# Kernel tuning notes

Measured on AMD Instinct MI355X. Metric: run time of the kernel, lower is better.

## Reference

```python
import jax, jax.numpy as jnp
import numpy as np

DN = ('NCHW', 'OIHW', 'NCHW')

def conv2d(x, w, b, stride, pad):
    y = jax.lax.conv_general_dilated(x, w, (stride, stride), ((pad, pad), (pad, pad)), dimension_numbers=DN)
    return y + b[None, :, None, None]

def convt2d(x, w, b):
    # torch ConvTranspose2d(k=4, stride=2, padding=1); torch weight layout [Cin, Cout, kH, kW]
    wf = jnp.flip(w, (2, 3)).transpose(1, 0, 2, 3)  # -> [Cout, Cin, kH, kW]
    y = jax.lax.conv_general_dilated(x, wf, (1, 1), ((2, 2), (2, 2)), lhs_dilation=(2, 2), dimension_numbers=DN)
    return y + b[None, :, None, None]

def setup_inputs() -> dict:
    key = jax.random.key(0)
    ks = jax.random.split(key, 20)
    Hc, E, K = 128, 256, 8192
    s = lambda k, shape, fan: jax.random.normal(k, shape, jnp.float32) * (1.0 / np.sqrt(fan))
    inp = {
        'x': jax.random.normal(ks[0], (4, 3, 256, 256), jnp.float32),
        'enc_w1': s(ks[1], (Hc, 3, 4, 4), 3 * 16), 'enc_b1': jnp.zeros((Hc,), jnp.float32),
        'enc_w2': s(ks[2], (Hc, Hc, 4, 4), Hc * 16), 'enc_b2': jnp.zeros((Hc,), jnp.float32),
        'enc_w3': s(ks[3], (Hc, Hc, 3, 3), Hc * 9), 'enc_b3': jnp.zeros((Hc,), jnp.float32),
        'qconv_w': s(ks[4], (E, Hc, 1, 1), Hc), 'qconv_b': jnp.zeros((E,), jnp.float32),
        'codebook': jax.random.uniform(ks[5], (K, E), jnp.float32, -1.0 / K, 1.0 / K),
        'pqconv_w': s(ks[6], (Hc, E, 1, 1), E), 'pqconv_b': jnp.zeros((Hc,), jnp.float32),
        'dec_w1': s(ks[7], (Hc, Hc, 3, 3), Hc * 9), 'dec_b1': jnp.zeros((Hc,), jnp.float32),
        'dect_w2': s(ks[8], (Hc, Hc, 4, 4), Hc * 16), 'dect_b2': jnp.zeros((Hc,), jnp.float32),
        'dect_w3': s(ks[9], (Hc, 3, 4, 4), Hc * 16), 'dect_b3': jnp.zeros((3,), jnp.float32),
    }
    return inp

def quantize(z, codebook):
    B, C, H, W = z.shape
    zf = z.transpose(0, 2, 3, 1).reshape(-1, C)  # [N, C]
    d = (jnp.sum(zf * zf, axis=1, keepdims=True)
         + jnp.sum(codebook * codebook, axis=1)
         - 2.0 * zf @ codebook.T)  # [N, K]
    indices = jnp.argmin(d, axis=1)
    quant = codebook[indices].reshape(B, H, W, C).transpose(0, 3, 1, 2)
    commit_loss = jnp.mean((jax.lax.stop_gradient(quant) - z) ** 2)
    quant = z + jax.lax.stop_gradient(quant - z)  # straight-through
    return quant, indices, commit_loss

def reference(x, enc_w1, enc_b1, enc_w2, enc_b2, enc_w3, enc_b3, qconv_w, qconv_b,
              codebook, pqconv_w, pqconv_b, dec_w1, dec_b1, dect_w2, dect_b2, dect_w3, dect_b3):
    h = jax.nn.relu(conv2d(x, enc_w1, enc_b1, 2, 1))
    h = jax.nn.relu(conv2d(h, enc_w2, enc_b2, 2, 1))
    h = conv2d(h, enc_w3, enc_b3, 1, 1)
    h = conv2d(h, qconv_w, qconv_b, 1, 0)
    quant, indices, commit_loss = quantize(h, codebook)
    q = conv2d(quant, pqconv_w, pqconv_b, 1, 0)
    d = jax.nn.relu(conv2d(q, dec_w1, dec_b1, 1, 1))
    d = jax.nn.relu(convt2d(d, dect_w2, dect_b2))
    recon = convt2d(d, dect_w3, dect_b3)
    return recon, commit_loss, indices
```

## Files before the change

### kernel.cpp

```cpp
#include <hip/hip_runtime.h>

#define OFF_A     ((size_t)0)
#define OFF_BINFO ((size_t)8388608)
#define OFF_B     ((size_t)34611200)
#define OFF_C     ((size_t)43532288)
#define OFF_D     ((size_t)52453376)
#define OFF_E     ((size_t)69230592)
#define OFF_ZN    ((size_t)81813504)
#define OFF_CN    ((size_t)81879040)
#define OFF_IDX   ((size_t)81911808)
#define OFF_ACC   ((size_t)81977344)
#define OFF_WR2   ((size_t)81977600)
#define OFF_WR3   ((size_t)83026176)
#define OFF_QWT   ((size_t)83050752)
#define OFF_WD2   ((size_t)83181824)
#define OFF_WD3   ((size_t)85278976)
#define OFF_WD1   ((size_t)86458624)

#define VQ_MARGIN 1.2e-4f
#define LDSS 40

typedef __attribute__((ext_vector_type(8))) _Float16 f16x8;
typedef __attribute__((ext_vector_type(4))) float f32x4;

__device__ __forceinline__ unsigned fkey(float f) {
  unsigned u = __float_as_uint(f);
  return (u & 0x80000000u) ? ~u : (u | 0x80000000u);
}
__device__ __forceinline__ float funkey(unsigned k) {
  unsigned u = (k & 0x80000000u) ? (k ^ 0x80000000u) : ~k;
  return __uint_as_float(u);
}
__device__ __forceinline__ void padzero_img(float* base, int S, int t) {
  for (int e = t; e < 4 * S - 4; e += 256) {
    int rr, cc;
    if (e < S) { rr = 0; cc = e; }
    else if (e < 2 * S) { rr = S - 1; cc = e - S; }
    else { rr = ((e - 2 * S) >> 1) + 1; cc = (e & 1) ? (S - 1) : 0; }
    base[rr * S + cc] = 0.0f;
  }
}

__global__ __launch_bounds__(256) void prep_k(
    const float* __restrict__ dtw2, float* __restrict__ wr2,
    const float* __restrict__ dtw3, float* __restrict__ wr3,
    const float* __restrict__ qw,   float* __restrict__ qwT,
    const float* __restrict__ ew2,  double* __restrict__ wd2,
    const float* __restrict__ ew3,  double* __restrict__ wd3,
    const float* __restrict__ ew1,  double* __restrict__ wd1,
    float* __restrict__ xpad, float* __restrict__ h1p, float* __restrict__ h2p) {
  int b = blockIdx.x, t = threadIdx.x;
  if (b < 256) {
    int tid = b * 256 + t;
    int ci = tid & 127, co = (tid >> 7) & 127, cls = tid >> 14;
    int kh0 = 1 - (cls >> 1), kw0 = 1 - (cls & 1);
    const float* s = dtw2 + ((size_t)ci * 128 + co) * 16;
    float* d = wr2 + (size_t)tid * 4;
    d[0] = s[kh0 * 4 + kw0];       d[1] = s[kh0 * 4 + kw0 + 2];
    d[2] = s[(kh0 + 2) * 4 + kw0]; d[3] = s[(kh0 + 2) * 4 + kw0 + 2];
  } else if (b < 262) {
    int tid = (b - 256) * 256 + t;
    if (tid < 1536) {
      int ci = tid & 127, co = (tid >> 7) % 3, cls = tid / 384;
      int kh0 = 1 - (cls >> 1), kw0 = 1 - (cls & 1);
      const float* s = dtw3 + ((size_t)ci * 3 + co) * 16;
      float* d = wr3 + (size_t)tid * 4;
      d[0] = s[kh0 * 4 + kw0];       d[1] = s[kh0 * 4 + kw0 + 2];
      d[2] = s[(kh0 + 2) * 4 + kw0]; d[3] = s[(kh0 + 2) * 4 + kw0 + 2];
    }
  } else if (b < 390) {
    int tid = (b - 262) * 256 + t;
    int co = tid & 255, ci = tid >> 8;
    qwT[(size_t)ci * 256 + co] = qw[(size_t)co * 128 + ci];
  } else if (b < 1414) {
    int tid = (b - 390) * 256 + t;
    wd2[tid] = (double)ew2[tid];
  } else if (b < 1990) {
    int tid = (b - 1414) * 256 + t;
    wd3[tid] = (double)ew3[tid];
  } else if (b < 2014) {
    int tid = (b - 1990) * 256 + t;
    wd1[tid] = (double)ew1[tid];
  } else if (b < 2026) {
    padzero_img(xpad + (size_t)(b - 2014) * 66564, 258, t);
  } else if (b < 2538) {
    padzero_img(h1p + (size_t)(b - 2026) * 16900, 130, t);
  } else {
    padzero_img(h2p + (size_t)(b - 2538) * 4356, 66, t);
  }
}

__global__ __launch_bounds__(256) void padx_k(const float* __restrict__ x,
                                              float* __restrict__ xp) {
  int tid = blockIdx.x * 256 + threadIdx.x;
  int wo = tid & 255, ho = (tid >> 8) & 255, c = tid >> 16;
  xp[((size_t)c * 258 + ho + 1) * 258 + wo + 1] = x[tid];
}

__global__ __launch_bounds__(256) void conv1_k(
    const float* __restrict__ xp, const double* __restrict__ wd,
    const float* __restrict__ bias, float* __restrict__ h1p) {
  int b = blockIdx.x;
  int chunk = b & 63, cog = (b >> 6) & 31, n = b >> 11;
  int t = threadIdx.x;
  int wo = t & 127, ho = chunk * 2 + (t >> 7);
  int co0 = cog * 4;
  const float* xb = xp + (size_t)n * 3 * 66564 + (size_t)(2 * ho) * 258 + 2 * wo;
  double acc[4] = {0.0, 0.0, 0.0, 0.0};
  for (int ci = 0; ci < 3; ++ci) {
    const float* xc = xb + (size_t)ci * 66564;
    double xd[16];
#pragma unroll
    for (int kh = 0; kh < 4; ++kh)
#pragma unroll
      for (int kw = 0; kw < 4; ++kw) xd[kh * 4 + kw] = (double)xc[kh * 258 + kw];
#pragma unroll
    for (int cc = 0; cc < 4; ++cc) {
      const double* wp = wd + (size_t)(co0 + cc) * 48 + ci * 16;
#pragma unroll
      for (int tp = 0; tp < 16; ++tp)
        acc[cc] = fma(xd[tp], wp[tp], acc[cc]);
    }
  }
#pragma unroll
  for (int cc = 0; cc < 4; ++cc) {
    float r = (float)((double)bias[co0 + cc] + acc[cc]);
    h1p[(((size_t)n * 128 + co0 + cc) * 130 + ho + 1) * 130 + wo + 1] = fmaxf(r, 0.0f);
  }
}

__global__ __launch_bounds__(256) void conv2_k(
    const float* __restrict__ h1p, const double* __restrict__ wd,
    const float* __restrict__ bias, float* __restrict__ h2p) {
  int b = blockIdx.x;
  int chunk = b & 15, cog = (b >> 4) & 31, n = b >> 9;
  int t = threadIdx.x;
  int wo = t & 63, ho = chunk * 4 + (t >> 6);
  int co0 = cog * 4;
  const float* xb = h1p + (size_t)n * 128 * 16900 + (size_t)(2 * ho) * 130 + 2 * wo;
  double acc[4] = {0.0, 0.0, 0.0, 0.0};
  for (int ci = 0; ci < 128; ++ci) {
    const float* xc = xb + (size_t)ci * 16900;
    double xd[16];
#pragma unroll
    for (int kh = 0; kh < 4; ++kh)
#pragma unroll
      for (int kw = 0; kw < 4; ++kw) xd[kh * 4 + kw] = (double)xc[kh * 130 + kw];
#pragma unroll
    for (int cc = 0; cc < 4; ++cc) {
      const double* wp = wd + (size_t)(co0 + cc) * 2048 + ci * 16;
#pragma unroll
      for (int tp = 0; tp < 16; ++tp)
        acc[cc] = fma(xd[tp], wp[tp], acc[cc]);
    }
  }
#pragma unroll
  for (int cc = 0; cc < 4; ++cc) {
    float r = (float)((double)bias[co0 + cc] + acc[cc]);
    h2p[(((size_t)n * 128 + co0 + cc) * 66 + ho + 1) * 66 + wo + 1] = fmaxf(r, 0.0f);
  }
}

__global__ __launch_bounds__(256) void conv3_k(
    const float* __restrict__ h2p, const double* __restrict__ wd,
    const float* __restrict__ bias, float* __restrict__ h3) {
  int b = blockIdx.x;
  int chunk = b & 15, cog = (b >> 4) & 31, n = b >> 9;
  int t = threadIdx.x;
  int wo = t & 63, ho = chunk * 4 + (t >> 6);
  int co0 = cog * 4;
  const float* xb = h2p + (size_t)n * 128 * 4356 + (size_t)ho * 66 + wo;
  double acc[4] = {0.0, 0.0, 0.0, 0.0};
  for (int ci = 0; ci < 128; ++ci) {
    const float* xc = xb + (size_t)ci * 4356;
    double xd[9];
#pragma unroll
    for (int kh = 0; kh < 3; ++kh)
#pragma unroll
      for (int kw = 0; kw < 3; ++kw) xd[kh * 3 + kw] = (double)xc[kh * 66 + kw];
#pragma unroll
    for (int cc = 0; cc < 4; ++cc) {
      const double* wp = wd + (size_t)(co0 + cc) * 1152 + ci * 9;
#pragma unroll
      for (int tp = 0; tp < 9; ++tp)
        acc[cc] = fma(xd[tp], wp[tp], acc[cc]);
    }
  }
#pragma unroll
  for (int cc = 0; cc < 4; ++cc)
    h3[(((size_t)n * 128 + co0 + cc) << 12) + (ho << 6) + wo] =
        (float)((double)bias[co0 + cc] + acc[cc]);
}

__global__ __launch_bounds__(256) void qconv_z_k(
    const float* __restrict__ h3, const float* __restrict__ wT,
    const float* __restrict__ bias, float* __restrict__ zf,
    _Float16* __restrict__ Ap, float* __restrict__ znb) {
  __shared__ double wsum[4];
  int p  = blockIdx.x;
  int co = threadIdx.x;
  int n  = p >> 12;
  int hw = p & 4095;
  const float* xp = h3 + ((size_t)n * 128) * 4096 + hw;
  double a[4] = {0.0, 0.0, 0.0, 0.0};
  for (int ci = 0; ci < 128; ci += 4) {
#pragma unroll
    for (int u = 0; u < 4; ++u) {
      float xv = xp[(size_t)(ci + u) * 4096];
      a[u] = fma((double)xv, (double)wT[(size_t)(ci + u) * 256 + co], a[u]);
    }
  }
  double acc = (double)bias[co] + ((a[0] + a[1]) + (a[2] + a[3]));
  float zv = (float)acc;
  zf[(size_t)p * 256 + co] = zv;
  Ap[(size_t)p * 256 + co] = (_Float16)zv;
  float xx = zv * zv;
  double s = (double)xx;
#pragma unroll
  for (int off = 32; off > 0; off >>= 1) s += __shfl_down(s, off, 64);
  if ((co & 63) == 0) wsum[co >> 6] = s;
  __syncthreads();
  if (co == 0) znb[p] = (float)((wsum[0] + wsum[1]) + (wsum[2] + wsum[3]));
}

__global__ __launch_bounds__(256) void cbprep_k(
    const float* __restrict__ cb, _Float16* __restrict__ Bp,
    float* __restrict__ cnb) {
  __shared__ double wsum[4];
  int k = blockIdx.x, t = threadIdx.x;
  float c = cb[(size_t)k * 256 + t];
  Bp[(size_t)k * 256 + t] = (_Float16)(c * 512.0f);
  float xx = c * c;
  double s = (double)xx;
#pragma unroll
  for (int off = 32; off > 0; off >>= 1) s += __shfl_down(s, off, 64);
  if ((t & 63) == 0) wsum[t >> 6] = s;
  __syncthreads();
  if (t == 0) cnb[k] = (float)((wsum[0] + wsum[1]) + (wsum[2] + wsum[3]));
}

__global__ __launch_bounds__(256, 2) void vq_gemm_k(
    const _Float16* __restrict__ Ah, const _Float16* __restrict__ Bh,
    const float* __restrict__ cnArr, int4* __restrict__ binfo) {
  __shared__ __align__(16) _Float16 As[128 * LDSS];
  __shared__ __align__(16) _Float16 Bs[128 * LDSS];
  __shared__ unsigned loc[128];
  __shared__ int cnt_sh[128];
  __shared__ int cand_sh[128][2];
  const int t = threadIdx.x;
  const int w = t >> 6, L = t & 63;
  const int mb = blockIdx.x >> 6;
  const int nb = blockIdx.x & 63;
  const int m0 = mb << 7, n0 = nb << 7;
  if (t < 128) { loc[t] = 0xFFFFFFFFu; cnt_sh[t] = 0; }
  f32x4 acc[4][4] = {};
  const int wr = (w >> 1) << 6, wc = (w & 1) << 6;
  const int srow = L >> 2, kg = L & 3;
  const int q = L >> 4, ln = L & 15;
  for (int kk = 0; kk < 256; kk += 32) {
    __syncthreads();
#pragma unroll
    for (int c = 0; c < 2; ++c) {
      const int row = (w << 5) + (c << 4) + srow;
      const f16x8 av = *(const f16x8*)(Ah + (size_t)(m0 + row) * 256 + kk + kg * 8);
      *(f16x8*)(&As[row * LDSS + kg * 8]) = av;
      const f16x8 bv = *(const f16x8*)(Bh + (size_t)(n0 + row) * 256 + kk + kg * 8);
      *(f16x8*)(&Bs[row * LDSS + kg * 8]) = bv;
    }
    __syncthreads();
    f16x8 af[4], bf[4];
#pragma unroll
    for (int i = 0; i < 4; ++i)
      af[i] = *(const f16x8*)(&As[(wr + 16 * i + ln) * LDSS + q * 8]);
#pragma unroll
    for (int j = 0; j < 4; ++j)
      bf[j] = *(const f16x8*)(&Bs[(wc + 16 * j + ln) * LDSS + q * 8]);
#pragma unroll
    for (int i = 0; i < 4; ++i)
#pragma unroll
      for (int j = 0; j < 4; ++j)
        acc[i][j] = __builtin_amdgcn_mfma_f32_16x16x32_f16(af[i], bf[j], acc[i][j], 0, 0, 0);
  }
  float cnv[4];
#pragma unroll
  for (int j = 0; j < 4; ++j) cnv[j] = cnArr[n0 + wc + 16 * j + ln];
#pragma unroll
  for (int i = 0; i < 4; ++i)
#pragma unroll
    for (int r = 0; r < 4; ++r) {
      float mn = 3.4e38f;
#pragma unroll
      for (int j = 0; j < 4; ++j)
        mn = fminf(mn, fmaf(-0.00390625f, acc[i][j][r], cnv[j]));
      atomicMin(&loc[wr + 16 * i + 4 * q + r], fkey(mn));
    }
  __syncthreads();
#pragma unroll
  for (int i = 0; i < 4; ++i)
#pragma unroll
    for (int r = 0; r < 4; ++r) {
      const int rib = wr + 16 * i + 4 * q + r;
      const float thr = funkey(loc[rib]) + VQ_MARGIN;
#pragma unroll
      for (int j = 0; j < 4; ++j) {
        float s = fmaf(-0.00390625f, acc[i][j][r], cnv[j]);
        if (s <= thr) {
          int slot = atomicAdd(&cnt_sh[rib], 1);
          if (slot < 2) cand_sh[rib][slot] = n0 + wc + 16 * j + ln;
        }
      }
    }
  __syncthreads();
  if (t < 128) {
    int4 v;
    v.x = cnt_sh[t];
    v.y = cand_sh[t][0];
    v.z = cand_sh[t][1];
    v.w = (int)__float_as_uint(funkey(loc[t]));
    binfo[(size_t)(m0 + t) * 64 + nb] = v;
  }
}

__global__ __launch_bounds__(256) void vq_phase3_k(
    const float* __restrict__ zf, const float* __restrict__ cb,
    const float* __restrict__ znArr, const float* __restrict__ cnArr,
    const int4* __restrict__ binfo, int* __restrict__ idxOut,
    float* __restrict__ accum) {
  if (blockIdx.x == 0 && threadIdx.x == 0) *accum = 0.0f;
  const int lane = threadIdx.x & 63;
  const int r = blockIdx.x * 4 + (threadIdx.x >> 6);
  const float* zr = zf + (size_t)r * 256;
  double z4[4];
#pragma unroll
  for (int j = 0; j < 4; ++j) z4[j] = (double)zr[lane + (j << 6)];
  const float znr = znArr[r];
  int4 b = binfo[(size_t)r * 64 + lane];
  float bv = __uint_as_float((unsigned)b.w);
  float m = bv;
#pragma unroll
  for (int off = 32; off > 0; off >>= 1) m = fminf(m, __shfl_down(m, off, 64));
  m = __shfl(m, 0, 64);
  const float thr = m + VQ_MARGIN;
  unsigned long long mask = __ballot(bv <= thr);
  float bestd = 3.4e38f;
  int bestk = 0x7fffffff;
  while (mask) {
    const int nb = (int)__builtin_ctzll(mask);
    mask &= mask - 1;
    const int c  = __shfl(b.x, nb, 64);
    const int k0 = __shfl(b.y, nb, 64);
    const int k1 = __shfl(b.z, nb, 64);
    const int nsc = (c <= 2) ? c : 128;
    for (int s2 = 0; s2 < nsc; ++s2) {
      const int k = (c <= 2) ? (s2 == 0 ? k0 : k1) : (nb * 128 + s2);
      const float* ck = cb + (size_t)k * 256;
      double p = 0.0;
#pragma unroll
      for (int j = 0; j < 4; ++j)
        p = fma(z4[j], (double)ck[lane + (j << 6)], p);
#pragma unroll
      for (int off = 32; off > 0; off >>= 1) p += __shfl_down(p, off, 64);
      if (lane == 0) {
        float mm2 = (float)(2.0 * p);
        float t1 = znr + cnArr[k];
        float d = t1 - mm2;
        if (d < bestd || (d == bestd && k < bestk)) { bestd = d; bestk = k; }
      }
    }
  }
  if (lane == 0) idxOut[r] = bestk;
}

__global__ __launch_bounds__(256) void commit_k(
    const float* __restrict__ zf, const float* __restrict__ cb,
    const int* __restrict__ idxArr, float* __restrict__ accum,
    float* __restrict__ outIdxF) {
  __shared__ float wsum[4];
  const int p = blockIdx.x;
  const int t = threadIdx.x;
  const int k = idxArr[p];
  float d = cb[(size_t)k * 256 + t] - zf[(size_t)p * 256 + t];
  float v = d * d;
#pragma unroll
  for (int off = 32; off > 0; off >>= 1) v += __shfl_down(v, off, 64);
  if ((t & 63) == 0) wsum[t >> 6] = v;
  __syncthreads();
  if (t == 0) {
    atomicAdd(accum, wsum[0] + wsum[1] + wsum[2] + wsum[3]);
    outIdxF[p] = (float)k;
  }
}

__global__ __launch_bounds__(256) void pc_k(const float* __restrict__ cb,
                                            const float* __restrict__ pw,
                                            float* __restrict__ PC) {
  int tid = blockIdx.x * 256 + threadIdx.x;
  int co = tid & 127, k = tid >> 7;
  const float* c = cb + (size_t)k * 256;
  const float* w = pw + (size_t)co * 256;
  float a0 = 0.0f, a1 = 0.0f, a2 = 0.0f, a3 = 0.0f;
  for (int ci = 0; ci < 256; ci += 4) {
    a0 = fmaf(c[ci], w[ci], a0);
    a1 = fmaf(c[ci + 1], w[ci + 1], a1);
    a2 = fmaf(c[ci + 2], w[ci + 2], a2);
    a3 = fmaf(c[ci + 3], w[ci + 3], a3);
  }
  PC[tid] = (a0 + a1) + (a2 + a3);
}

__global__ __launch_bounds__(256) void padzero_dec_k(
    float* __restrict__ qbufp, float* __restrict__ d1p, float* __restrict__ d2p) {
  int b = blockIdx.x, t = threadIdx.x;
  if (b < 512)       padzero_img(qbufp + (size_t)b * 4356, 66, t);
  else if (b < 1024) padzero_img(d1p + (size_t)(b - 512) * 4356, 66, t);
  else               padzero_img(d2p + (size_t)(b - 1024) * 16900, 130, t);
}

__global__ __launch_bounds__(256) void gather_pc_k(
    const float* __restrict__ PC, const int* __restrict__ idxArr,
    const float* __restrict__ pb, float* __restrict__ qp) {
  int tid = blockIdx.x * 256 + threadIdx.x;
  int hw = tid & 4095;
  int co = (tid >> 12) & 127;
  int n  = tid >> 19;
  int p  = (n << 12) + hw;
  int h = hw >> 6, w2 = hw & 63;
  qp[(((size_t)n * 128 + co) * 66 + h + 1) * 66 + w2 + 1] =
      PC[(size_t)idxArr[p] * 128 + co] + pb[co];
}

__global__ __launch_bounds__(256) void dconv1_k(
    const float* __restrict__ qp, const float* __restrict__ w,
    const float* __restrict__ bias, float* __restrict__ d1p) {
  int b = blockIdx.x;
  int chunk = b & 15, cog = (b >> 4) & 31, n = b >> 9;
  int t = threadIdx.x;
  int wo = t & 63, ho = chunk * 4 + (t >> 6);
  int co0 = cog * 4;
  const float* xb = qp + (size_t)n * 128 * 4356 + (size_t)ho * 66 + wo;
  float acc[4] = {0.0f, 0.0f, 0.0f, 0.0f};
  for (int ci = 0; ci < 128; ++ci) {
    const float* xc = xb + (size_t)ci * 4356;
    float xv[9];
#pragma unroll
    for (int kh = 0; kh < 3; ++kh)
#pragma unroll
      for (int kw = 0; kw < 3; ++kw) xv[kh * 3 + kw] = xc[kh * 66 + kw];
#pragma unroll
    for (int cc = 0; cc < 4; ++cc) {
      const float* wp = w + (size_t)(co0 + cc) * 1152 + ci * 9;
#pragma unroll
      for (int tp = 0; tp < 9; ++tp)
        acc[cc] = fmaf(xv[tp], wp[tp], acc[cc]);
    }
  }
#pragma unroll
  for (int cc = 0; cc < 4; ++cc)
    d1p[(((size_t)n * 128 + co0 + cc) * 66 + ho + 1) * 66 + wo + 1] =
        fmaxf(bias[co0 + cc] + acc[cc], 0.0f);
}

__global__ __launch_bounds__(256) void convt2_k(
    const float* __restrict__ xp, const float* __restrict__ wr,
    const float* __restrict__ bias, float* __restrict__ y) {
  int b = blockIdx.x;
  int chunk = b & 15, cls = (b >> 4) & 3, cog = (b >> 6) & 31, n = b >> 11;
  int cph = cls >> 1, cpw = cls & 1;
  int t = threadIdx.x;
  int wb = t & 63, i = chunk * 4 + (t >> 6);
  int co0 = cog * 4;
  int ho = 2 * i + cph, wo = 2 * wb + cpw;
  int r0 = i + 1 + cph, r1 = r0 - 1;
  int c0 = wb + 1 + cpw, c1 = c0 - 1;
  const float* xb = xp + (size_t)n * 128 * 4356;
  float acc[4] = {0.0f, 0.0f, 0.0f, 0.0f};
  for (int ci = 0; ci < 128; ++ci) {
    const float* xc = xb + (size_t)ci * 4356;
    float x00 = xc[r0 * 66 + c0], x01 = xc[r0 * 66 + c1];
    float x10 = xc[r1 * 66 + c0], x11 = xc[r1 * 66 + c1];
#pragma unroll
    for (int cc = 0; cc < 4; ++cc) {
      const float* w4 = wr + (((size_t)cls * 128 + co0 + cc) * 128 + ci) * 4;
      acc[cc] = fmaf(x00, w4[0], acc[cc]);
      acc[cc] = fmaf(x01, w4[1], acc[cc]);
      acc[cc] = fmaf(x10, w4[2], acc[cc]);
      acc[cc] = fmaf(x11, w4[3], acc[cc]);
    }
  }
#pragma unroll
  for (int cc = 0; cc < 4; ++cc)
    y[(((size_t)n * 128 + co0 + cc) * 130 + ho + 1) * 130 + wo + 1] =
        fmaxf(bias[co0 + cc] + acc[cc], 0.0f);
}

__global__ __launch_bounds__(256) void convt3_k(
    const float* __restrict__ xp, const float* __restrict__ wr,
    const float* __restrict__ bias, float* __restrict__ y,
    const float* __restrict__ accum, float* __restrict__ outLoss) {
  int b = blockIdx.x;
  if (b == 0 && threadIdx.x == 0) *outLoss = *accum * (1.0f / 4194304.0f);
  int chunk = b & 63, cls = (b >> 6) & 3, n = b >> 8;
  int cph = cls >> 1, cpw = cls & 1;
  int t = threadIdx.x;
  int wb = t & 127, i = chunk * 2 + (t >> 7);
  int ho = 2 * i + cph, wo = 2 * wb + cpw;
  int r0 = i + 1 + cph, r1 = r0 - 1;
  int c0 = wb + 1 + cpw, c1 = c0 - 1;
  const float* xb = xp + (size_t)n * 128 * 16900;
  float acc[3] = {0.0f, 0.0f, 0.0f};
  for (int ci = 0; ci < 128; ++ci) {
    const float* xc = xb + (size_t)ci * 16900;
    float x00 = xc[r0 * 130 + c0], x01 = xc[r0 * 130 + c1];
    float x10 = xc[r1 * 130 + c0], x11 = xc[r1 * 130 + c1];
#pragma unroll
    for (int cc = 0; cc < 3; ++cc) {
      const float* w4 = wr + (((size_t)cls * 3 + cc) * 128 + ci) * 4;
      acc[cc] = fmaf(x00, w4[0], acc[cc]);
      acc[cc] = fmaf(x01, w4[1], acc[cc]);
      acc[cc] = fmaf(x10, w4[2], acc[cc]);
      acc[cc] = fmaf(x11, w4[3], acc[cc]);
    }
  }
#pragma unroll
  for (int cc = 0; cc < 3; ++cc)
    y[(((size_t)n * 3 + cc) << 16) + (ho << 8) + wo] = bias[cc] + acc[cc];
}

extern "C" void kernel_launch(void* const* d_in, const int* in_sizes, int n_in,
                              void* d_out, int out_size, void* d_ws, size_t ws_size,
                              hipStream_t stream) {
  const float* x    = (const float*)d_in[0];
  const float* ew1  = (const float*)d_in[1];
  const float* eb1  = (const float*)d_in[2];
  const float* ew2  = (const float*)d_in[3];
  const float* eb2  = (const float*)d_in[4];
  const float* ew3  = (const float*)d_in[5];
  const float* eb3  = (const float*)d_in[6];
  const float* qw   = (const float*)d_in[7];
  const float* qb   = (const float*)d_in[8];
  const float* cb   = (const float*)d_in[9];
  const float* pw   = (const float*)d_in[10];
  const float* pb   = (const float*)d_in[11];
  const float* dw1  = (const float*)d_in[12];
  const float* db1  = (const float*)d_in[13];
  const float* dtw2 = (const float*)d_in[14];
  const float* dtb2 = (const float*)d_in[15];
  const float* dtw3 = (const float*)d_in[16];
  const float* dtb3 = (const float*)d_in[17];

  char* wsb = (char*)d_ws;
  float*    h1p  = (float*)(wsb + OFF_A);
  _Float16* Ap   = (_Float16*)(wsb + OFF_A);
  int4*     binfo= (int4*)(wsb + OFF_BINFO);
  float*    d2p  = (float*)(wsb + OFF_A);
  float*    h2p  = (float*)(wsb + OFF_B);
  float*    qbufp= (float*)(wsb + OFF_B);
  float*    xpad = (float*)(wsb + OFF_C);
  float*    h3   = (float*)(wsb + OFF_C);
  float*    d1p  = (float*)(wsb + OFF_C);
  float*    zff  = (float*)(wsb + OFF_D);
  _Float16* Bp   = (_Float16*)(wsb + OFF_E);
  float*    PC   = (float*)(wsb + OFF_E);
  float*    znb  = (float*)(wsb + OFF_ZN);
  float*    cnb  = (float*)(wsb + OFF_CN);
  int*      idxb = (int*)(wsb + OFF_IDX);
  float*    accum= (float*)(wsb + OFF_ACC);
  float*    wr2  = (float*)(wsb + OFF_WR2);
  float*    wr3  = (float*)(wsb + OFF_WR3);
  float*    qwT  = (float*)(wsb + OFF_QWT);
  double*   wd2  = (double*)(wsb + OFF_WD2);
  double*   wd3  = (double*)(wsb + OFF_WD3);
  double*   wd1  = (double*)(wsb + OFF_WD1);

  float* out      = (float*)d_out;
  float* outLoss  = out + 786432;
  float* outIdxF  = out + 786433;

  hipLaunchKernelGGL(prep_k, dim3(3050), dim3(256), 0, stream,
                     dtw2, wr2, dtw3, wr3, qw, qwT, ew2, wd2, ew3, wd3,
                     ew1, wd1, xpad, h1p, h2p);

  hipLaunchKernelGGL(padx_k,    dim3(3072),  dim3(256), 0, stream, x, xpad);
  hipLaunchKernelGGL(conv1_k,   dim3(8192),  dim3(256), 0, stream, xpad, wd1, eb1, h1p);
  hipLaunchKernelGGL(conv2_k,   dim3(2048),  dim3(256), 0, stream, h1p, wd2, eb2, h2p);
  hipLaunchKernelGGL(conv3_k,   dim3(2048),  dim3(256), 0, stream, h2p, wd3, eb3, h3);
  hipLaunchKernelGGL(qconv_z_k, dim3(16384), dim3(256), 0, stream, h3, qwT, qb, zff, Ap, znb);

  hipLaunchKernelGGL(cbprep_k,    dim3(8192),  dim3(256), 0, stream, cb, Bp, cnb);
  hipLaunchKernelGGL(vq_gemm_k,   dim3(8192),  dim3(256), 0, stream, Ap, Bp, cnb, binfo);
  hipLaunchKernelGGL(vq_phase3_k, dim3(4096),  dim3(256), 0, stream, zff, cb, znb, cnb, binfo, idxb, accum);
  hipLaunchKernelGGL(commit_k,    dim3(16384), dim3(256), 0, stream, zff, cb, idxb, accum, outIdxF);

  hipLaunchKernelGGL(pc_k,          dim3(4096), dim3(256), 0, stream, cb, pw, PC);
  hipLaunchKernelGGL(padzero_dec_k, dim3(1536), dim3(256), 0, stream, qbufp, d1p, d2p);
  hipLaunchKernelGGL(gather_pc_k,   dim3(8192), dim3(256), 0, stream, PC, idxb, pb, qbufp);
  hipLaunchKernelGGL(dconv1_k,      dim3(2048), dim3(256), 0, stream, qbufp, dw1, db1, d1p);
  hipLaunchKernelGGL(convt2_k,      dim3(8192), dim3(256), 0, stream, d1p, wr2, dtb2, d2p);
  hipLaunchKernelGGL(convt3_k,      dim3(1024), dim3(256), 0, stream, d2p, wr3, dtb3, out, accum, outLoss);
}
```

Measured before the change: 1.540 ms.

## Prefetch conv inputs, interleave weights by output group, and remap blocks per XCD

Double-precision encoder weights are rearranged so the four output channels of a group sit next to each other, letting each input value feed four contiguous weight loads. The direct-conv kernels (conv2, conv3, dconv1, convt2, convt3) now software-prefetch the next input channel's patch into registers while computing the current one. Block indices are remapped so blocks sharing the same spatial tile land on the same XCD for L2 reuse, and launch bounds request 4 blocks per CU. The cost is higher register pressure from the prefetch buffers, which may cause spills or lower occupancy under the min-blocks hint.

Result: slower. 1.603 ms (+4.0%).

```diff
diff --git a/kernel.cpp b/kernel.cpp
--- a/kernel.cpp
+++ b/kernel.cpp
@@ -74,13 +74,18 @@
     qwT[(size_t)ci * 256 + co] = qw[(size_t)co * 128 + ci];
   } else if (b < 1414) {
     int tid = (b - 390) * 256 + t;
-    wd2[tid] = (double)ew2[tid];
+    int co = tid >> 11, ci = (tid >> 4) & 127, tp = tid & 15;
+    wd2[((((size_t)(co >> 2) * 128 + ci) * 16 + tp) << 2) + (co & 3)] = (double)ew2[tid];
   } else if (b < 1990) {
     int tid = (b - 1414) * 256 + t;
-    wd3[tid] = (double)ew3[tid];
+    int co = tid / 1152, rem = tid - co * 1152;
+    int ci = rem / 9, tp = rem - ci * 9;
+    wd3[((((size_t)(co >> 2) * 128 + ci) * 9 + tp) << 2) + (co & 3)] = (double)ew3[tid];
   } else if (b < 2014) {
     int tid = (b - 1990) * 256 + t;
-    wd1[tid] = (double)ew1[tid];
+    int co = tid / 48, rem = tid - co * 48;
+    int ci = rem >> 4, tp = rem & 15;
+    wd1[((((size_t)(co >> 2) * 3 + ci) * 16 + tp) << 2) + (co & 3)] = (double)ew1[tid];
   } else if (b < 2026) {
     padzero_img(xpad + (size_t)(b - 2014) * 66564, 258, t);
   } else if (b < 2538) {
@@ -97,7 +102,7 @@
   xp[((size_t)c * 258 + ho + 1) * 258 + wo + 1] = x[tid];
 }
 
-__global__ __launch_bounds__(256) void conv1_k(
+__global__ __launch_bounds__(256, 4) void conv1_k(
     const float* __restrict__ xp, const double* __restrict__ wd,
     const float* __restrict__ bias, float* __restrict__ h1p) {
   int b = blockIdx.x;
@@ -106,22 +111,26 @@
   int wo = t & 127, ho = chunk * 2 + (t >> 7);
   int co0 = cog * 4;
   const float* xb = xp + (size_t)n * 3 * 66564 + (size_t)(2 * ho) * 258 + 2 * wo;
-  double acc[4] = {0.0, 0.0, 0.0, 0.0};
+  const double* wb = wd + (size_t)cog * 192;
+  float cf[48];
+#pragma unroll
   for (int ci = 0; ci < 3; ++ci) {
     const float* xc = xb + (size_t)ci * 66564;
-    double xd[16];
 #pragma unroll
     for (int kh = 0; kh < 4; ++kh)
 #pragma unroll
-      for (int kw = 0; kw < 4; ++kw) xd[kh * 4 + kw] = (double)xc[kh * 258 + kw];
-#pragma unroll
-    for (int cc = 0; cc < 4; ++cc) {
-      const double* wp = wd + (size_t)(co0 + cc) * 48 + ci * 16;
-#pragma unroll
-      for (int tp = 0; tp < 16; ++tp)
-        acc[cc] = fma(xd[tp], wp[tp], acc[cc]);
-    }
-  }
+      for (int kw = 0; kw < 4; ++kw) cf[ci * 16 + kh * 4 + kw] = xc[kh * 258 + kw];
+  }
+  double acc[4] = {0.0, 0.0, 0.0, 0.0};
+#pragma unroll
+  for (int ci = 0; ci < 3; ++ci)
+#pragma unroll
+    for (int tp = 0; tp < 16; ++tp) {
+      double xd = (double)cf[ci * 16 + tp];
+      const double* w4 = wb + ((size_t)ci * 16 + tp) * 4;
+#pragma unroll
+      for (int cc = 0; cc < 4; ++cc) acc[cc] = fma(xd, w4[cc], acc[cc]);
+    }
 #pragma unroll
   for (int cc = 0; cc < 4; ++cc) {
     float r = (float)((double)bias[co0 + cc] + acc[cc]);
@@ -129,30 +138,41 @@
   }
 }
 
-__global__ __launch_bounds__(256) void conv2_k(
+__global__ __launch_bounds__(256, 4) void conv2_k(
     const float* __restrict__ h1p, const double* __restrict__ wd,
     const float* __restrict__ bias, float* __restrict__ h2p) {
-  int b = blockIdx.x;
-  int chunk = b & 15, cog = (b >> 4) & 31, n = b >> 9;
+  int bid = blockIdx.x;
+  int xcd = bid & 7, slot = bid >> 3;
+  int g = xcd * 8 + (slot >> 5);
+  int cog = slot & 31;
+  int n = g >> 4, chunk = g & 15;
   int t = threadIdx.x;
   int wo = t & 63, ho = chunk * 4 + (t >> 6);
   int co0 = cog * 4;
   const float* xb = h1p + (size_t)n * 128 * 16900 + (size_t)(2 * ho) * 130 + 2 * wo;
+  const double* wb = wd + (size_t)cog * 8192;
   double acc[4] = {0.0, 0.0, 0.0, 0.0};
+  float cf[16], nf[16];
+#pragma unroll
+  for (int kh = 0; kh < 4; ++kh)
+#pragma unroll
+    for (int kw = 0; kw < 4; ++kw) cf[kh * 4 + kw] = xb[kh * 130 + kw];
   for (int ci = 0; ci < 128; ++ci) {
-    const float* xc = xb + (size_t)ci * 16900;
-    double xd[16];
+    const float* xn = xb + (size_t)((ci + 1) & 127) * 16900;
 #pragma unroll
     for (int kh = 0; kh < 4; ++kh)
 #pragma unroll
-      for (int kw = 0; kw < 4; ++kw) xd[kh * 4 + kw] = (double)xc[kh * 130 + kw];
-#pragma unroll
-    for (int cc = 0; cc < 4; ++cc) {
-      const double* wp = wd + (size_t)(co0 + cc) * 2048 + ci * 16;
-#pragma unroll
-      for (int tp = 0; tp < 16; ++tp)
-        acc[cc] = fma(xd[tp], wp[tp], acc[cc]);
-    }
+      for (int kw = 0; kw < 4; ++kw) nf[kh * 4 + kw] = xn[kh * 130 + kw];
+    const double* wp = wb + (size_t)ci * 64;
+#pragma unroll
+    for (int tp = 0; tp < 16; ++tp) {
+      double xd = (double)cf[tp];
+#pragma unroll
+      for (int cc = 0; cc < 4; ++cc)
+        acc[cc] = fma(xd, wp[tp * 4 + cc], acc[cc]);
+    }
+#pragma unroll
+    for (int q = 0; q < 16; ++q) cf[q] = nf[q];
   }
 #pragma unroll
   for (int cc = 0; cc < 4; ++cc) {
@@ -161,30 +181,41 @@
   }
 }
 
-__global__ __launch_bounds__(256) void conv3_k(
+__global__ __launch_bounds__(256, 4) void conv3_k(
     const float* __restrict__ h2p, const double* __restrict__ wd,
     const float* __restrict__ bias, float* __restrict__ h3) {
-  int b = blockIdx.x;
-  int chunk = b & 15, cog = (b >> 4) & 31, n = b >> 9;
+  int bid = blockIdx.x;
+  int xcd = bid & 7, slot = bid >> 3;
+  int g = xcd * 8 + (slot >> 5);
+  int cog = slot & 31;
+  int n = g >> 4, chunk = g & 15;
   int t = threadIdx.x;
   int wo = t & 63, ho = chunk * 4 + (t >> 6);
   int co0 = cog * 4;
   const float* xb = h2p + (size_t)n * 128 * 4356 + (size_t)ho * 66 + wo;
+  const double* wb = wd + (size_t)cog * 4608;
   double acc[4] = {0.0, 0.0, 0.0, 0.0};
+  float cf[9], nf[9];
+#pragma unroll
+  for (int kh = 0; kh < 3; ++kh)
+#pragma unroll
+    for (int kw = 0; kw < 3; ++kw) cf[kh * 3 + kw] = xb[kh * 66 + kw];
   for (int ci = 0; ci < 128; ++ci) {
-    const float* xc = xb + (size_t)ci * 4356;
-    double xd[9];
+    const float* xn = xb + (size_t)((ci + 1) & 127) * 4356;
 #pragma unroll
     for (int kh = 0; kh < 3; ++kh)
 #pragma unroll
-      for (int kw = 0; kw < 3; ++kw) xd[kh * 3 + kw] = (double)xc[kh * 66 + kw];
-#pragma unroll
-    for (int cc = 0; cc < 4; ++cc) {
-      const double* wp = wd + (size_t)(co0 + cc) * 1152 + ci * 9;
-#pragma unroll
-      for (int tp = 0; tp < 9; ++tp)
-        acc[cc] = fma(xd[tp], wp[tp], acc[cc]);
-    }
+      for (int kw = 0; kw < 3; ++kw) nf[kh * 3 + kw] = xn[kh * 66 + kw];
+    const double* wp = wb + (size_t)ci * 36;
+#pragma unroll
+    for (int tp = 0; tp < 9; ++tp) {
+      double xd = (double)cf[tp];
+#pragma unroll
+      for (int cc = 0; cc < 4; ++cc)
+        acc[cc] = fma(xd, wp[tp * 4 + cc], acc[cc]);
+    }
+#pragma unroll
+    for (int q = 0; q < 9; ++q) cf[q] = nf[q];
   }
 #pragma unroll
   for (int cc = 0; cc < 4; ++cc)
@@ -429,30 +460,39 @@
       PC[(size_t)idxArr[p] * 128 + co] + pb[co];
 }
 
-__global__ __launch_bounds__(256) void dconv1_k(
+__global__ __launch_bounds__(256, 4) void dconv1_k(
     const float* __restrict__ qp, const float* __restrict__ w,
     const float* __restrict__ bias, float* __restrict__ d1p) {
-  int b = blockIdx.x;
-  int chunk = b & 15, cog = (b >> 4) & 31, n = b >> 9;
+  int bid = blockIdx.x;
+  int xcd = bid & 7, slot = bid >> 3;
+  int g = xcd * 8 + (slot >> 5);
+  int cog = slot & 31;
+  int n = g >> 4, chunk = g & 15;
   int t = threadIdx.x;
   int wo = t & 63, ho = chunk * 4 + (t >> 6);
   int co0 = cog * 4;
   const float* xb = qp + (size_t)n * 128 * 4356 + (size_t)ho * 66 + wo;
   float acc[4] = {0.0f, 0.0f, 0.0f, 0.0f};
+  float cf[9], nf[9];
+#pragma unroll
+  for (int kh = 0; kh < 3; ++kh)
+#pragma unroll
+    for (int kw = 0; kw < 3; ++kw) cf[kh * 3 + kw] = xb[kh * 66 + kw];
   for (int ci = 0; ci < 128; ++ci) {
-    const float* xc = xb + (size_t)ci * 4356;
-    float xv[9];
+    const float* xn = xb + (size_t)((ci + 1) & 127) * 4356;
 #pragma unroll
     for (int kh = 0; kh < 3; ++kh)
 #pragma unroll
-      for (int kw = 0; kw < 3; ++kw) xv[kh * 3 + kw] = xc[kh * 66 + kw];
+      for (int kw = 0; kw < 3; ++kw) nf[kh * 3 + kw] = xn[kh * 66 + kw];
 #pragma unroll
     for (int cc = 0; cc < 4; ++cc) {
       const float* wp = w + (size_t)(co0 + cc) * 1152 + ci * 9;
 #pragma unroll
       for (int tp = 0; tp < 9; ++tp)
-        acc[cc] = fmaf(xv[tp], wp[tp], acc[cc]);
-    }
+        acc[cc] = fmaf(cf[tp], wp[tp], acc[cc]);
+    }
+#pragma unroll
+    for (int q = 0; q < 9; ++q) cf[q] = nf[q];
   }
 #pragma unroll
   for (int cc = 0; cc < 4; ++cc)
@@ -460,32 +500,53 @@
         fmaxf(bias[co0 + cc] + acc[cc], 0.0f);
 }
 
-__global__ __launch_bounds__(256) void convt2_k(
+__global__ __launch_bounds__(256, 4) void convt2_k(
     const float* __restrict__ xp, const float* __restrict__ wr,
     const float* __restrict__ bias, float* __restrict__ y) {
-  int b = blockIdx.x;
-  int chunk = b & 15, cls = (b >> 4) & 3, cog = (b >> 6) & 31, n = b >> 11;
+  int bid = blockIdx.x;
+  int xcd = bid & 7, slot = bid >> 3;
+  int g = xcd * 8 + (slot >> 7);
+  int inner = slot & 127;
+  int cog = inner & 31, cls = (inner >> 5) & 3;
+  int n = g >> 4, chunk = g & 15;
   int cph = cls >> 1, cpw = cls & 1;
   int t = threadIdx.x;
-  int wb = t & 63, i = chunk * 4 + (t >> 6);
+  int wl = t & 63, i = chunk * 4 + (t >> 6);
   int co0 = cog * 4;
-  int ho = 2 * i + cph, wo = 2 * wb + cpw;
+  int ho = 2 * i + cph, wo = 2 * wl + cpw;
   int r0 = i + 1 + cph, r1 = r0 - 1;
-  int c0 = wb + 1 + cpw, c1 = c0 - 1;
+  int c0 = wl + 1 + cpw, c1 = c0 - 1;
   const float* xb = xp + (size_t)n * 128 * 4356;
   float acc[4] = {0.0f, 0.0f, 0.0f, 0.0f};
-  for (int ci = 0; ci < 128; ++ci) {
-    const float* xc = xb + (size_t)ci * 4356;
-    float x00 = xc[r0 * 66 + c0], x01 = xc[r0 * 66 + c1];
-    float x10 = xc[r1 * 66 + c0], x11 = xc[r1 * 66 + c1];
-#pragma unroll
-    for (int cc = 0; cc < 4; ++cc) {
-      const float* w4 = wr + (((size_t)cls * 128 + co0 + cc) * 128 + ci) * 4;
-      acc[cc] = fmaf(x00, w4[0], acc[cc]);
-      acc[cc] = fmaf(x01, w4[1], acc[cc]);
-      acc[cc] = fmaf(x10, w4[2], acc[cc]);
-      acc[cc] = fmaf(x11, w4[3], acc[cc]);
-    }
+  float cur[16], nxt[16];
+#pragma unroll
+  for (int u = 0; u < 4; ++u) {
+    const float* xc = xb + (size_t)u * 4356;
+    cur[u * 4 + 0] = xc[r0 * 66 + c0]; cur[u * 4 + 1] = xc[r0 * 66 + c1];
+    cur[u * 4 + 2] = xc[r1 * 66 + c0]; cur[u * 4 + 3] = xc[r1 * 66 + c1];
+  }
+  for (int ci4 = 0; ci4 < 128; ci4 += 4) {
+    int nb4 = (ci4 + 4) & 127;
+#pragma unroll
+    for (int u = 0; u < 4; ++u) {
+      const float* xc = xb + (size_t)(nb4 + u) * 4356;
+      nxt[u * 4 + 0] = xc[r0 * 66 + c0]; nxt[u * 4 + 1] = xc[r0 * 66 + c1];
+      nxt[u * 4 + 2] = xc[r1 * 66 + c0]; nxt[u * 4 + 3] = xc[r1 * 66 + c1];
+    }
+#pragma unroll
+    for (int u = 0; u < 4; ++u) {
+      int ci = ci4 + u;
+#pragma unroll
+      for (int cc = 0; cc < 4; ++cc) {
+        const float* w4 = wr + (((size_t)cls * 128 + co0 + cc) * 128 + ci) * 4;
+        acc[cc] = fmaf(cur[u * 4 + 0], w4[0], acc[cc]);
+        acc[cc] = fmaf(cur[u * 4 + 1], w4[1], acc[cc]);
+        acc[cc] = fmaf(cur[u * 4 + 2], w4[2], acc[cc]);
+        acc[cc] = fmaf(cur[u * 4 + 3], w4[3], acc[cc]);
+      }
+    }
+#pragma unroll
+    for (int q = 0; q < 16; ++q) cur[q] = nxt[q];
   }
 #pragma unroll
   for (int cc = 0; cc < 4; ++cc)
@@ -493,33 +554,53 @@
         fmaxf(bias[co0 + cc] + acc[cc], 0.0f);
 }
 
-__global__ __launch_bounds__(256) void convt3_k(
+__global__ __launch_bounds__(256, 4) void convt3_k(
     const float* __restrict__ xp, const float* __restrict__ wr,
     const float* __restrict__ bias, float* __restrict__ y,
     const float* __restrict__ accum, float* __restrict__ outLoss) {
-  int b = blockIdx.x;
-  if (b == 0 && threadIdx.x == 0) *outLoss = *accum * (1.0f / 4194304.0f);
-  int chunk = b & 63, cls = (b >> 6) & 3, n = b >> 8;
+  int bid = blockIdx.x;
+  if (bid == 0 && threadIdx.x == 0) *outLoss = *accum * (1.0f / 4194304.0f);
+  int xcd = bid & 7, slot = bid >> 3;
+  int g = xcd * 32 + (slot >> 2);
+  int cls = slot & 3;
+  int n = g >> 6, chunk = g & 63;
   int cph = cls >> 1, cpw = cls & 1;
   int t = threadIdx.x;
-  int wb = t & 127, i = chunk * 2 + (t >> 7);
-  int ho = 2 * i + cph, wo = 2 * wb + cpw;
+  int wl = t & 127, i = chunk * 2 + (t >> 7);
+  int ho = 2 * i + cph, wo = 2 * wl + cpw;
   int r0 = i + 1 + cph, r1 = r0 - 1;
-  int c0 = wb + 1 + cpw, c1 = c0 - 1;
+  int c0 = wl + 1 + cpw, c1 = c0 - 1;
   const float* xb = xp + (size_t)n * 128 * 16900;
   float acc[3] = {0.0f, 0.0f, 0.0f};
-  for (int ci = 0; ci < 128; ++ci) {
-    const float* xc = xb + (size_t)ci * 16900;
-    float x00 = xc[r0 * 130 + c0], x01 = xc[r0 * 130 + c1];
-    float x10 = xc[r1 * 130 + c0], x11 = xc[r1 * 130 + c1];
-#pragma unroll
-    for (int cc = 0; cc < 3; ++cc) {
-      const float* w4 = wr + (((size_t)cls * 3 + cc) * 128 + ci) * 4;
-      acc[cc] = fmaf(x00, w4[0], acc[cc]);
-      acc[cc] = fmaf(x01, w4[1], acc[cc]);
-      acc[cc] = fmaf(x10, w4[2], acc[cc]);
-      acc[cc] = fmaf(x11, w4[3], acc[cc]);
-    }
+  float cur[16], nxt[16];
+#pragma unroll
+  for (int u = 0; u < 4; ++u) {
+    const float* xc = xb + (size_t)u * 16900;
+    cur[u * 4 + 0] = xc[r0 * 130 + c0]; cur[u * 4 + 1] = xc[r0 * 130 + c1];
+    cur[u * 4 + 2] = xc[r1 * 130 + c0]; cur[u * 4 + 3] = xc[r1 * 130 + c1];
+  }
+  for (int ci4 = 0; ci4 < 128; ci4 += 4) {
+    int nb4 = (ci4 + 4) & 127;
+#pragma unroll
+    for (int u = 0; u < 4; ++u) {
+      const float* xc = xb + (size_t)(nb4 + u) * 16900;
+      nxt[u * 4 + 0] = xc[r0 * 130 + c0]; nxt[u * 4 + 1] = xc[r0 * 130 + c1];
+      nxt[u * 4 + 2] = xc[r1 * 130 + c0]; nxt[u * 4 + 3] = xc[r1 * 130 + c1];
+    }
+#pragma unroll
+    for (int u = 0; u < 4; ++u) {
+      int ci = ci4 + u;
+#pragma unroll
+      for (int cc = 0; cc < 3; ++cc) {
+        const float* w4 = wr + (((size_t)cls * 3 + cc) * 128 + ci) * 4;
+        acc[cc] = fmaf(cur[u * 4 + 0], w4[0], acc[cc]);
+        acc[cc] = fmaf(cur[u * 4 + 1], w4[1], acc[cc]);
+        acc[cc] = fmaf(cur[u * 4 + 2], w4[2], acc[cc]);
+        acc[cc] = fmaf(cur[u * 4 + 3], w4[3], acc[cc]);
+      }
+    }
+#pragma unroll
+    for (int q = 0; q < 16; ++q) cur[q] = nxt[q];
   }
 #pragma unroll
   for (int cc = 0; cc < 3; ++cc)
```
